# Kernel optimization log

Measured on AMD Instinct MI355X. Metric: run time of the kernel, lower is better.

## Reference

```python
import jax, jax.numpy as jnp
import numpy as np

TAGSET = 128
B, T = 128, 1024


def setup_inputs() -> dict:
    key = jax.random.key(0)
    k1, k2, k3, k4, k5 = jax.random.split(key, 5)
    feats = jax.random.normal(k1, (B, T, TAGSET), dtype=jnp.float32)
    tags = jax.random.randint(k2, (B, T), 0, TAGSET, dtype=jnp.int64)
    mask = jnp.ones((B, T), dtype=bool)
    transitions = 0.01 * jax.random.normal(k3, (TAGSET, TAGSET), dtype=jnp.float32)
    start_transitions = 0.01 * jax.random.normal(k4, (TAGSET,), dtype=jnp.float32)
    stop_transitions = 0.01 * jax.random.normal(k5, (TAGSET,), dtype=jnp.float32)
    return {"feats": feats, "transitions": transitions,
            "start_transitions": start_transitions, "stop_transitions": stop_transitions,
            "tags": tags, "mask": mask}


def _forward_alg(feats, transitions, start_transitions, stop_transitions, mask):
    # feats: [B,T,K], mask: [B,T]
    fv0 = start_transitions + feats[:, 0]  # [B,K]

    def step(fv, xs):
        feat_t, mask_t = xs  # [B,K], [B]
        # prev-tag axis is last: fv[b, j] + transitions[i, j] + feat_t[b, i]
        score = fv[:, None, :] + transitions[None, :, :] + feat_t[:, :, None]  # [B,K,K]
        nxt = jax.nn.logsumexp(score, axis=-1)  # [B,K]
        fv = jnp.where(mask_t[:, None], nxt, fv)
        return fv, None

    xs = (jnp.swapaxes(feats[:, 1:], 0, 1), jnp.swapaxes(mask[:, 1:], 0, 1))
    fv, _ = jax.lax.scan(step, fv0, xs)
    return jax.nn.logsumexp(fv + stop_transitions, axis=-1)  # [B]


def _score_sentence(feats, transitions, start_transitions, stop_transitions, tags, mask):
    b, t = mask.shape
    trans_score = transitions[tags[:, 1:], tags[:, :-1]]  # [B,T-1]
    emit = jnp.take_along_axis(feats, tags[:, :, None], axis=2)[..., 0]  # [B,T]
    score = jnp.where(mask[:, 1:], trans_score + emit[:, 1:], 0.0).sum(-1)
    score = score + emit[:, 0] + start_transitions[tags[:, 0]]
    last_idx = mask.astype(jnp.int32).sum(-1) - 1  # [B]
    last_tags = tags[jnp.arange(b), last_idx]
    return score + stop_transitions[last_tags]


def reference(feats, transitions, start_transitions, stop_transitions, tags, mask):
    fwd = _forward_alg(feats, transitions, start_transitions, stop_transitions, mask)
    gold = _score_sentence(feats, transitions, start_transitions, stop_transitions, tags, mask)
    return (fwd - gold).mean()
```

## Files before the change

### kernel.cpp

```cpp
#include <hip/hip_runtime.h>
#include <hip/hip_bf16.h>

#define T_LEN 1024
#define NT 128
#define CHUNK 32
#define NCHUNK (T_LEN / CHUNK)

__device__ __forceinline__ void bar_lds() {
  asm volatile("s_waitcnt lgkmcnt(0)" ::: "memory");
  __builtin_amdgcn_s_barrier();
}

__device__ __forceinline__ unsigned short f2bf(float x) {
  __hip_bfloat16 h = __float2bfloat16(x);
  return *reinterpret_cast<unsigned short*>(&h);
}
__device__ __forceinline__ float bf_lo(unsigned int d) {
  return __uint_as_float(d << 16);
}
__device__ __forceinline__ float bf_hi(unsigned int d) {
  return __uint_as_float(d & 0xffff0000u);
}

__device__ __forceinline__ void gload16(const float* g, float* l) {
  __builtin_amdgcn_global_load_lds(
      (const __attribute__((address_space(1))) unsigned int*)g,
      (__attribute__((address_space(3))) unsigned int*)l, 16, 0, 0);
}

__global__ __launch_bounds__(256, 1) void crf_forward_kernel(
    const float* __restrict__ feats, const float* __restrict__ trans,
    const float* __restrict__ start, const float* __restrict__ stop,
    float* __restrict__ fwd_out) {
  const int b = blockIdx.x;
  const int tid = (int)threadIdx.x;
  const int lane = tid & 63;
  const int w = tid >> 6;
  const int l15 = lane & 15;
  const int q = lane >> 4;
  const int j0 = 16 * w + l15;
  const int jw = j0 + ((lane & 16) ? 64 : 0);

  alignas(16) __shared__ unsigned short pbuf[2][NT];
  alignas(16) __shared__ float fstage[2][CHUNK * NT];
  __shared__ float wred[4];

  const float* fb = feats + (size_t)b * T_LEN * NT;

#define STAGE(c, buf)                                                   \
  {                                                                     \
    _Pragma("unroll") for (int seg = 0; seg < 4; ++seg) {               \
      const float* g = fb + (c) * (CHUNK * NT) + seg * 1024 + tid * 4;  \
      float* l = &fstage[buf][seg * 1024 + w * 256];                    \
      gload16(g, l);                                                    \
    }                                                                   \
  }
  STAGE(0, 0)
  STAGE(1, 1)

  float E0[32], E1[32];
#pragma unroll
  for (int n = 0; n < 8; ++n) {
    float4 t0 =
        *reinterpret_cast<const float4*>(&trans[j0 * NT + 32 * q + 4 * n]);
    float4 t1 = *reinterpret_cast<const float4*>(
        &trans[(j0 + 64) * NT + 32 * q + 4 * n]);
    E0[4 * n + 0] = __expf(t0.x); E0[4 * n + 1] = __expf(t0.y);
    E0[4 * n + 2] = __expf(t0.z); E0[4 * n + 3] = __expf(t0.w);
    E1[4 * n + 0] = __expf(t1.x); E1[4 * n + 1] = __expf(t1.y);
    E1[4 * n + 2] = __expf(t1.z); E1[4 * n + 3] = __expf(t1.w);
  }

  float base = start[0] + fb[0];
  if (tid < NT) pbuf[0][tid] = f2bf(__expf(start[tid] + fb[tid] - base));
  float C = base;

  int cur = 0;

#define STEP(fcur, trow)                                                   \
  {                                                                        \
    const unsigned short* pb = &pbuf[cur][q * 32];                         \
    float u0 = bf_lo((unsigned int)pbuf[cur][0]);                          \
    float f_me = fstage[fcur][(trow) * NT + jw];                           \
    float f_0 = fstage[fcur][(trow) * NT];                                 \
    float a00 = 0.f, a01 = 0.f, a10 = 0.f, a11 = 0.f;                      \
    _Pragma("unroll") for (int n = 0; n < 4; ++n) {                        \
      uint4 d4 = *reinterpret_cast<const uint4*>(pb + 8 * n);              \
      {                                                                    \
        float lo = bf_lo(d4.x), hi = bf_hi(d4.x);                          \
        a00 = fmaf(lo, E0[8 * n + 0], a00);                                \
        a01 = fmaf(hi, E0[8 * n + 1], a01);                                \
        a10 = fmaf(lo, E1[8 * n + 0], a10);                                \
        a11 = fmaf(hi, E1[8 * n + 1], a11);                                \
      }                                                                    \
      {                                                                    \
        float lo = bf_lo(d4.y), hi = bf_hi(d4.y);                          \
        a00 = fmaf(lo, E0[8 * n + 2], a00);                                \
        a01 = fmaf(hi, E0[8 * n + 3], a01);                                \
        a10 = fmaf(lo, E1[8 * n + 2], a10);                                \
        a11 = fmaf(hi, E1[8 * n + 3], a11);                                \
      }                                                                    \
      {                                                                    \
        float lo = bf_lo(d4.z), hi = bf_hi(d4.z);                          \
        a00 = fmaf(lo, E0[8 * n + 4], a00);                                \
        a01 = fmaf(hi, E0[8 * n + 5], a01);                                \
        a10 = fmaf(lo, E1[8 * n + 4], a10);                                \
        a11 = fmaf(hi, E1[8 * n + 5], a11);                                \
      }                                                                    \
      {                                                                    \
        float lo = bf_lo(d4.w), hi = bf_hi(d4.w);                          \
        a00 = fmaf(lo, E0[8 * n + 6], a00);                                \
        a01 = fmaf(hi, E0[8 * n + 7], a01);                                \
        a10 = fmaf(lo, E1[8 * n + 6], a10);                                \
        a11 = fmaf(hi, E1[8 * n + 7], a11);                                \
      }                                                                    \
    }                                                                      \
    float eterm = __expf(f_me - f_0);                                      \
    float re = __builtin_amdgcn_rcpf(u0) * eterm;                          \
    float s0 = a00 + a01;                                                  \
    s0 += __shfl_xor(s0, 16);                                              \
    s0 += __shfl_xor(s0, 32);                                              \
    float s1 = a10 + a11;                                                  \
    s1 += __shfl_xor(s1, 16);                                              \
    s1 += __shfl_xor(s1, 32);                                              \
    float sv = (lane & 16) ? s1 : s0;                                      \
    float unew = sv * re;                                                  \
    if (lane < 32) pbuf[cur ^ 1][jw] = f2bf(unew);                         \
    C += __logf(u0) + f_0;                                                 \
    bar_lds();                                                             \
    cur ^= 1;                                                              \
  }

  asm volatile("s_waitcnt vmcnt(4)" ::: "memory");
  bar_lds();

#pragma unroll 4
  for (int trow = 1; trow < CHUNK; ++trow) STEP(0, trow)

  for (int c = 1; c < NCHUNK; ++c) {
    if (c + 1 < NCHUNK) {
      STAGE(c + 1, (c + 1) & 1)
      asm volatile("s_waitcnt vmcnt(4)" ::: "memory");
    } else {
      asm volatile("s_waitcnt vmcnt(0)" ::: "memory");
    }
    __builtin_amdgcn_s_barrier();
    const int fcur = c & 1;
#pragma unroll 4
    for (int trow = 0; trow < CHUNK; ++trow) STEP(fcur, trow)
  }
#undef STEP
#undef STAGE

  float val = (tid < NT)
                  ? bf_lo((unsigned int)pbuf[cur][tid]) * __expf(stop[tid])
                  : 0.f;
#pragma unroll
  for (int off = 1; off <= 32; off <<= 1) val += __shfl_xor(val, off);
  if (lane == 0) wred[w] = val;
  bar_lds();
  if (tid == 0) {
    float tot = (wred[0] + wred[1]) + (wred[2] + wred[3]);
    fwd_out[b] = C + __logf(tot);
  }
}

__global__ __launch_bounds__(256) void crf_gold_kernel(
    const float* __restrict__ feats, const float* __restrict__ trans,
    const float* __restrict__ start, const float* __restrict__ stop,
    const int* __restrict__ tags, const float* __restrict__ fwd,
    float* __restrict__ diff) {
  const int b = blockIdx.x;
  const int tid = (int)threadIdx.x;
  const int lane = tid & 63;
  const int w = tid >> 6;
  const int* tg = tags + b * T_LEN;
  const float* fb = feats + (size_t)b * T_LEN * NT;

  float acc = 0.f;
  for (int s = tid; s < T_LEN; s += 256) {
    int cu = tg[s];
    acc += fb[s * NT + cu];
    if (s > 0) acc += trans[cu * NT + tg[s - 1]];
  }
#pragma unroll
  for (int off = 1; off <= 32; off <<= 1) acc += __shfl_xor(acc, off);
  __shared__ float wr[4];
  if (lane == 0) wr[w] = acc;
  __syncthreads();
  if (tid == 0) {
    float gold = (wr[0] + wr[1]) + (wr[2] + wr[3]) + start[tg[0]] +
                 stop[tg[T_LEN - 1]];
    diff[b] = fwd[b] - gold;
  }
}

__global__ __launch_bounds__(128) void crf_final_kernel(
    const float* __restrict__ diff, float* __restrict__ out) {
  const int tid = (int)threadIdx.x;
  const int lane = tid & 63;
  const int w = tid >> 6;
  float v = diff[tid];
#pragma unroll
  for (int off = 1; off <= 32; off <<= 1) v += __shfl_xor(v, off);
  __shared__ float wr[2];
  if (lane == 0) wr[w] = v;
  __syncthreads();
  if (tid == 0) out[0] = (wr[0] + wr[1]) * (1.0f / 128.0f);
}

extern "C" void kernel_launch(void* const* d_in, const int* in_sizes, int n_in,
                              void* d_out, int out_size, void* d_ws,
                              size_t ws_size, hipStream_t stream) {
  const float* feats = (const float*)d_in[0];
  const float* trans = (const float*)d_in[1];
  const float* start = (const float*)d_in[2];
  const float* stop = (const float*)d_in[3];
  const int* tags = (const int*)d_in[4];
  float* ws = (float*)d_ws;
  float* fwd = ws;
  float* diff = ws + 128;
  float* out = (float*)d_out;

  crf_forward_kernel<<<128, 256, 0, stream>>>(feats, trans, start, stop, fwd);
  crf_gold_kernel<<<128, 256, 0, stream>>>(feats, trans, start, stop, tags, fwd,
                                           diff);
  crf_final_kernel<<<1, 128, 0, stream>>>(diff, out);
}
```

Baseline: 491.6 us.

## Interleave four sequences per block in CRF forward recurrence

Each forward block now processes four batch sequences at once. Their per-timestep steps are interleaved so that a single LDS barrier covers all four, and there is more independent work per step to hide latency. The feature staging chunk shrinks to 8 rows per sequence, and the final log-sum-exp uses one wave per sequence. The grid shrinks to a quarter of the blocks. Each block still walks the full serial chain of 1024 steps but does four times the work per step, so far fewer CUs are used.

```diff
diff --git a/kernel.cpp b/kernel.cpp
--- a/kernel.cpp
+++ b/kernel.cpp
@@ -3,7 +3,8 @@
 
 #define T_LEN 1024
 #define NT 128
-#define CHUNK 32
+#define SEQ 4
+#define CHUNK 8
 #define NCHUNK (T_LEN / CHUNK)
 
 __device__ __forceinline__ void bar_lds() {
@@ -32,7 +33,7 @@
     const float* __restrict__ feats, const float* __restrict__ trans,
     const float* __restrict__ start, const float* __restrict__ stop,
     float* __restrict__ fwd_out) {
-  const int b = blockIdx.x;
+  const int b0 = blockIdx.x * SEQ;
   const int tid = (int)threadIdx.x;
   const int lane = tid & 63;
   const int w = tid >> 6;
@@ -41,22 +42,22 @@
   const int j0 = 16 * w + l15;
   const int jw = j0 + ((lane & 16) ? 64 : 0);
 
-  alignas(16) __shared__ unsigned short pbuf[2][NT];
-  alignas(16) __shared__ float fstage[2][CHUNK * NT];
-  __shared__ float wred[4];
-
-  const float* fb = feats + (size_t)b * T_LEN * NT;
-
-#define STAGE(c, buf)                                                   \
-  {                                                                     \
-    _Pragma("unroll") for (int seg = 0; seg < 4; ++seg) {               \
-      const float* g = fb + (c) * (CHUNK * NT) + seg * 1024 + tid * 4;  \
-      float* l = &fstage[buf][seg * 1024 + w * 256];                    \
-      gload16(g, l);                                                    \
-    }                                                                   \
-  }
-  STAGE(0, 0)
-  STAGE(1, 1)
+  alignas(16) __shared__ unsigned short pbuf[SEQ][2][NT];
+  alignas(16) __shared__ float fstage[SEQ][2][CHUNK * NT];
+  __shared__ float wred_unused[4];
+  (void)wred_unused;
+
+  const float* fb[SEQ];
+#pragma unroll
+  for (int s = 0; s < SEQ; ++s) fb[s] = feats + (size_t)(b0 + s) * T_LEN * NT;
+
+#define STAGE(s, c, buf) \
+  gload16(fb[s] + (c) * (CHUNK * NT) + tid * 4, &fstage[s][buf][tid * 4]);
+
+#pragma unroll
+  for (int s = 0; s < SEQ; ++s) STAGE(s, 0, 0)
+#pragma unroll
+  for (int s = 0; s < SEQ; ++s) STAGE(s, 1, 1)
 
   float E0[32], E1[32];
 #pragma unroll
@@ -71,18 +72,22 @@
     E1[4 * n + 2] = __expf(t1.z); E1[4 * n + 3] = __expf(t1.w);
   }
 
-  float base = start[0] + fb[0];
-  if (tid < NT) pbuf[0][tid] = f2bf(__expf(start[tid] + fb[tid] - base));
-  float C = base;
+  float C[SEQ];
+#pragma unroll
+  for (int s = 0; s < SEQ; ++s) {
+    float base = start[0] + fb[s][0];
+    if (tid < NT) pbuf[s][0][tid] = f2bf(__expf(start[tid] + fb[s][tid] - base));
+    C[s] = base;
+  }
 
   int cur = 0;
 
-#define STEP(fcur, trow)                                                   \
+#define STEP(s, fc, trow)                                                  \
   {                                                                        \
-    const unsigned short* pb = &pbuf[cur][q * 32];                         \
-    float u0 = bf_lo((unsigned int)pbuf[cur][0]);                          \
-    float f_me = fstage[fcur][(trow) * NT + jw];                           \
-    float f_0 = fstage[fcur][(trow) * NT];                                 \
+    const unsigned short* pb = &pbuf[s][cur][q * 32];                      \
+    float u0 = bf_lo((unsigned int)pbuf[s][cur][0]);                       \
+    float f_me = fstage[s][fc][(trow) * NT + jw];                          \
+    float f_0 = fstage[s][fc][(trow) * NT];                                \
     float a00 = 0.f, a01 = 0.f, a10 = 0.f, a11 = 0.f;                      \
     _Pragma("unroll") for (int n = 0; n < 4; ++n) {                        \
       uint4 d4 = *reinterpret_cast<const uint4*>(pb + 8 * n);              \
@@ -125,43 +130,46 @@
     s1 += __shfl_xor(s1, 32);                                              \
     float sv = (lane & 16) ? s1 : s0;                                      \
     float unew = sv * re;                                                  \
-    if (lane < 32) pbuf[cur ^ 1][jw] = f2bf(unew);                         \
-    C += __logf(u0) + f_0;                                                 \
-    bar_lds();                                                             \
-    cur ^= 1;                                                              \
+    if (lane < 32) pbuf[s][cur ^ 1][jw] = f2bf(unew);                      \
+    C[s] += __logf(u0) + f_0;                                              \
   }
 
   asm volatile("s_waitcnt vmcnt(4)" ::: "memory");
   bar_lds();
 
-#pragma unroll 4
-  for (int trow = 1; trow < CHUNK; ++trow) STEP(0, trow)
+  for (int trow = 1; trow < CHUNK; ++trow) {
+    STEP(0, 0, trow) STEP(1, 0, trow) STEP(2, 0, trow) STEP(3, 0, trow)
+    bar_lds();
+    cur ^= 1;
+  }
 
   for (int c = 1; c < NCHUNK; ++c) {
     if (c + 1 < NCHUNK) {
-      STAGE(c + 1, (c + 1) & 1)
+#pragma unroll
+      for (int s = 0; s < SEQ; ++s) STAGE(s, c + 1, (c + 1) & 1)
       asm volatile("s_waitcnt vmcnt(4)" ::: "memory");
     } else {
       asm volatile("s_waitcnt vmcnt(0)" ::: "memory");
     }
     __builtin_amdgcn_s_barrier();
-    const int fcur = c & 1;
-#pragma unroll 4
-    for (int trow = 0; trow < CHUNK; ++trow) STEP(fcur, trow)
+    const int fc = c & 1;
+    for (int trow = 0; trow < CHUNK; ++trow) {
+      STEP(0, fc, trow) STEP(1, fc, trow) STEP(2, fc, trow) STEP(3, fc, trow)
+      bar_lds();
+      cur ^= 1;
+    }
   }
 #undef STEP
 #undef STAGE
 
-  float val = (tid < NT)
-                  ? bf_lo((unsigned int)pbuf[cur][tid]) * __expf(stop[tid])
-                  : 0.f;
-#pragma unroll
-  for (int off = 1; off <= 32; off <<= 1) val += __shfl_xor(val, off);
-  if (lane == 0) wred[w] = val;
-  bar_lds();
-  if (tid == 0) {
-    float tot = (wred[0] + wred[1]) + (wred[2] + wred[3]);
-    fwd_out[b] = C + __logf(tot);
+  {
+    float v0 = bf_lo((unsigned int)pbuf[w][cur][lane]) * __expf(stop[lane]);
+    float v1 =
+        bf_lo((unsigned int)pbuf[w][cur][lane + 64]) * __expf(stop[lane + 64]);
+    float val = v0 + v1;
+#pragma unroll
+    for (int off = 1; off <= 32; off <<= 1) val += __shfl_xor(val, off);
+    if (lane == 0) fwd_out[b0 + w] = C[w] + __logf(val);
   }
 }
 
@@ -222,7 +230,8 @@
   float* diff = ws + 128;
   float* out = (float*)d_out;
 
-  crf_forward_kernel<<<128, 256, 0, stream>>>(feats, trans, start, stop, fwd);
+  crf_forward_kernel<<<128 / SEQ, 256, 0, stream>>>(feats, trans, start, stop,
+                                                    fwd);
   crf_gold_kernel<<<128, 256, 0, stream>>>(feats, trans, start, stop, tags, fwd,
                                            diff);
   crf_final_kernel<<<1, 128, 0, stream>>>(diff, out);
```

Result: slower. 1.815 ms (+269.1%).
